# Kernel optimization log

Measured on AMD Instinct MI355X. Metric: run time of the kernel, lower is better.

Reference implementation:

```python
import jax, jax.numpy as jnp
import numpy as np

B, N, C, C_OUT, E = 8, 1024, 256, 256, 16384


def setup_inputs() -> dict:
    key = jax.random.key(0)
    k1, k2, k3 = jax.random.split(key, 3)
    x = jax.random.normal(k1, (B, N, C), dtype=jnp.float32)
    edge_index = jax.random.randint(k2, (2, E, B), 0, N)  # [2, E, B], values in [0, N)
    W = jax.random.normal(k3, (C_OUT, C), dtype=jnp.float32) * 0.02  # torch Linear weight [out, in]
    b = jnp.zeros((C_OUT,), dtype=jnp.float32)
    return {"x": x, "edge_index": edge_index, "W": W, "b": b}


def reference(x, edge_index, W, b):
    Bs, Nn, Cc = x.shape
    BN = Bs * Nn
    # Vectorized version of the per-batch python loop: offset each graph's
    # node indices into the big block-diagonal adjacency.
    offs = jnp.arange(Bs, dtype=edge_index.dtype) * Nn          # [B]
    src = (edge_index[0] + offs[None, :]).reshape(-1)           # [E*B]
    dst = (edge_index[1] + offs[None, :]).reshape(-1)           # [E*B]
    adj = jnp.zeros((BN, BN), dtype=x.dtype).at[src, dst].set(1.0)
    adj = adj + jnp.eye(BN, dtype=x.dtype)                      # self loops (adds on top, as in torch code)
    D = adj.sum(axis=1)                                         # [BN]
    d_inv_sqrt = jnp.where(D > 0, jax.lax.rsqrt(D), 0.0)        # pow(-0.5) with inf -> 0
    adj_n = d_inv_sqrt[:, None] * adj * d_inv_sqrt[None, :]     # D^-1/2 A D^-1/2
    h = adj_n @ x.reshape(BN, Cc)                               # [BN, C]
    out = h @ W.T + b                                           # Linear
    return out.reshape(Bs, Nn, -1)
```

## Files before the change

### kernel.cpp

```cpp
#include <hip/hip_runtime.h>
#include <stdint.h>

#define B_   8
#define N_   1024
#define C_   256
#define E_   16384
#define BN_  (B_ * N_)
#define NW_  (N_ / 32)
#define LIST_CAP 96

typedef __attribute__((ext_vector_type(8))) short bf16x8;
typedef __attribute__((ext_vector_type(4))) float f32x4;

static __device__ __forceinline__ short f32_to_bf16(float f) {
  uint32_t u = __float_as_uint(f);
  uint32_t r = (u + 0x7fffu + ((u >> 16) & 1u)) >> 16;
  return (short)r;
}
static __device__ __forceinline__ float bf16_to_f32(short s) {
  return __uint_as_float(((uint32_t)(uint16_t)s) << 16);
}

__global__ __launch_bounds__(256) void scatter_edges(
    const int* __restrict__ ei, uint32_t* __restrict__ mask) {
  int t = blockIdx.x * 256 + threadIdx.x;
  if (t >= E_ * B_) return;
  int b   = t & (B_ - 1);
  int src = ei[t];
  int dst = ei[E_ * B_ + t];
  int row = b * N_ + src;
  atomicOr(&mask[row * NW_ + (dst >> 5)], 1u << (dst & 31));
}

__global__ __launch_bounds__(256) void gemm_bf16x3(
    const float* __restrict__ X, const float* __restrict__ W,
    const uint32_t* __restrict__ mask, float* __restrict__ Z) {
  __shared__ __attribute__((aligned(16))) short Ah[64][40];
  __shared__ __attribute__((aligned(16))) short Al[64][40];
  __shared__ __attribute__((aligned(16))) short Bh[64][40];
  __shared__ __attribute__((aligned(16))) short Bl[64][40];
  __shared__ int   dpart[4][64];
  __shared__ float dinv_s[64];

  int t  = threadIdx.x;
  int m0 = blockIdx.x * 64;
  int n0 = blockIdx.y * 64;

  {
    int row = t & 63, part = t >> 6;
    const uint4* mp =
        (const uint4*)&mask[(size_t)(m0 + row) * NW_ + part * 8];
    uint4 a = mp[0], b = mp[1];
    dpart[part][row] = __popc(a.x) + __popc(a.y) + __popc(a.z) + __popc(a.w) +
                       __popc(b.x) + __popc(b.y) + __popc(b.z) + __popc(b.w);
  }
  __syncthreads();
  if (t < 64) {
    int d = dpart[0][t] + dpart[1][t] + dpart[2][t] + dpart[3][t] + 1;
    dinv_s[t] = rsqrtf((float)d);
  }

  int lr = t >> 2;
  int lc = (t & 3) * 8;
  int wv = t >> 6;
  int ln = t & 63;
  int lm = ln & 15;
  int qd = ln >> 4;

  f32x4 acc[4];
#pragma unroll
  for (int i = 0; i < 4; i++) acc[i] = (f32x4){0.f, 0.f, 0.f, 0.f};

  for (int k0 = 0; k0 < C_; k0 += 32) {
    const float* xr = &X[(size_t)(m0 + lr) * C_ + k0 + lc];
    const float* wr = &W[(size_t)(n0 + lr) * C_ + k0 + lc];
    float xv[8], wv8[8];
    *(float4*)&xv[0] = *(const float4*)&xr[0];
    *(float4*)&xv[4] = *(const float4*)&xr[4];
    *(float4*)&wv8[0] = *(const float4*)&wr[0];
    *(float4*)&wv8[4] = *(const float4*)&wr[4];
    bf16x8 xh, xl, wh, wl;
#pragma unroll
    for (int j = 0; j < 8; j++) {
      short h = f32_to_bf16(xv[j]);
      xh[j] = h;
      xl[j] = f32_to_bf16(xv[j] - bf16_to_f32(h));
      short g = f32_to_bf16(wv8[j]);
      wh[j] = g;
      wl[j] = f32_to_bf16(wv8[j] - bf16_to_f32(g));
    }
    __syncthreads();
    *(bf16x8*)&Ah[lr][lc] = xh;
    *(bf16x8*)&Al[lr][lc] = xl;
    *(bf16x8*)&Bh[lr][lc] = wh;
    *(bf16x8*)&Bl[lr][lc] = wl;
    __syncthreads();

    bf16x8 ah = *(const bf16x8*)&Ah[16 * wv + lm][qd * 8];
    bf16x8 al = *(const bf16x8*)&Al[16 * wv + lm][qd * 8];
#pragma unroll
    for (int nt = 0; nt < 4; nt++) {
      bf16x8 bh = *(const bf16x8*)&Bh[nt * 16 + lm][qd * 8];
      bf16x8 bl = *(const bf16x8*)&Bl[nt * 16 + lm][qd * 8];
      acc[nt] = __builtin_amdgcn_mfma_f32_16x16x32_bf16(ah, bh, acc[nt], 0, 0, 0);
      acc[nt] = __builtin_amdgcn_mfma_f32_16x16x32_bf16(ah, bl, acc[nt], 0, 0, 0);
      acc[nt] = __builtin_amdgcn_mfma_f32_16x16x32_bf16(al, bh, acc[nt], 0, 0, 0);
    }
  }
  __syncthreads();

  float di[4];
#pragma unroll
  for (int r = 0; r < 4; r++) di[r] = dinv_s[16 * wv + qd * 4 + r];
#pragma unroll
  for (int nt = 0; nt < 4; nt++) {
#pragma unroll
    for (int r = 0; r < 4; r++) {
      int m = m0 + 16 * wv + qd * 4 + r;
      int n = n0 + nt * 16 + lm;
      Z[(size_t)m * C_ + n] = di[r] * acc[nt][r];
    }
  }
}

__global__ __launch_bounds__(256) void aggregate(
    const uint32_t* __restrict__ mask, const float* __restrict__ Z,
    const float* __restrict__ bias, float* __restrict__ out) {
  __shared__ uint16_t lists[4][LIST_CAP];

  int blk   = blockIdx.x;
  int batch = blk & 7;
  int group = blk >> 3;
  int wv    = threadIdx.x >> 6;
  int ln    = threadIdx.x & 63;
  int loc   = group * 4 + wv;
  int node  = batch * N_ + loc;
  int c4    = ln * 4;

  uint32_t bits = (ln < NW_) ? mask[(size_t)node * NW_ + ln] : 0u;
  int cnt = __popc(bits);
  int pfx = cnt;
#pragma unroll
  for (int off = 1; off < 64; off <<= 1) {
    int v = __shfl_up(pfx, off);
    if (ln >= off) pfx += v;
  }
  int total = __shfl(pfx, 63);
  pfx -= cnt;
  uint16_t* lst = lists[wv];
  int o = pfx, jb = ln * 32;
  while (bits) {
    int j = __ffs(bits) - 1;
    bits &= bits - 1;
    lst[o++] = (uint16_t)(jb + j);
  }
  if (ln == 0) {
    int dd = total;
    while (dd & 3) lst[dd++] = 0;
  }

  const float* zb = Z + (size_t)batch * N_ * C_;
  float4 acc = *(const float4*)&zb[(size_t)loc * C_ + c4];

  for (int k = 0; k < total; k += 4) {
    ushort4 n4 = *(const ushort4*)&lst[k];
    float4 z0 = *(const float4*)&zb[(size_t)n4.x * C_ + c4];
    float4 z1 = *(const float4*)&zb[(size_t)n4.y * C_ + c4];
    float4 z2 = *(const float4*)&zb[(size_t)n4.z * C_ + c4];
    float4 z3 = *(const float4*)&zb[(size_t)n4.w * C_ + c4];
    float w1 = (k + 1 < total) ? 1.f : 0.f;
    float w2 = (k + 2 < total) ? 1.f : 0.f;
    float w3 = (k + 3 < total) ? 1.f : 0.f;
    acc.x += z0.x; acc.y += z0.y; acc.z += z0.z; acc.w += z0.w;
    acc.x += w1 * z1.x; acc.y += w1 * z1.y; acc.z += w1 * z1.z; acc.w += w1 * z1.w;
    acc.x += w2 * z2.x; acc.y += w2 * z2.y; acc.z += w2 * z2.z; acc.w += w2 * z2.w;
    acc.x += w3 * z3.x; acc.y += w3 * z3.y; acc.z += w3 * z3.z; acc.w += w3 * z3.w;
  }

  float di = rsqrtf((float)(total + 1));
  float4 bb = *(const float4*)&bias[c4];
  float4 o4;
  o4.x = di * acc.x + bb.x;
  o4.y = di * acc.y + bb.y;
  o4.z = di * acc.z + bb.z;
  o4.w = di * acc.w + bb.w;
  *(float4*)&out[(size_t)node * C_ + c4] = o4;
}

extern "C" void kernel_launch(void* const* d_in, const int* in_sizes, int n_in,
                              void* d_out, int out_size, void* d_ws,
                              size_t ws_size, hipStream_t stream) {
  const float* x    = (const float*)d_in[0];
  const int*   ei   = (const int*)d_in[1];
  const float* W    = (const float*)d_in[2];
  const float* bias = (const float*)d_in[3];
  float*       out  = (float*)d_out;

  char* ws = (char*)d_ws;
  uint32_t* mask = (uint32_t*)(ws + 0x000000);
  float*    Z    = (float*)   (ws + 0x100000);

  hipMemsetAsync(mask, 0, (size_t)BN_ * NW_ * 4, stream);

  scatter_edges<<<(E_ * B_) / 256, 256, 0, stream>>>(ei, mask);
  gemm_bf16x3<<<dim3(BN_ / 64, C_ / 64), 256, 0, stream>>>(x, W, mask, Z);
  aggregate<<<BN_ / 4, 256, 0, stream>>>(mask, Z, bias, out);
}
```

Baseline: 97.17 us.

## Preload whole W tile to LDS once and load X fragments directly into registers

The GEMM kernel now converts the block's full 64x256 slice of W into bf16 hi/lo parts and stores it in shared memory once, in a k-chunk-major layout. Each wave then loads its X fragments straight from global memory into MFMA operand registers, which removes the A tiles from LDS and the two barriers per k-step. The grid becomes 1D with a remapped block index so that blocks sharing an X row tile are interleaved. LDS use grows to about 64KB per block, which can cut occupancy, and X reads are now uncoalesced per-lane 32-byte loads.

```diff
diff --git a/kernel.cpp b/kernel.cpp
--- a/kernel.cpp
+++ b/kernel.cpp
@@ -35,16 +35,17 @@
 __global__ __launch_bounds__(256) void gemm_bf16x3(
     const float* __restrict__ X, const float* __restrict__ W,
     const uint32_t* __restrict__ mask, float* __restrict__ Z) {
-  __shared__ __attribute__((aligned(16))) short Ah[64][40];
-  __shared__ __attribute__((aligned(16))) short Al[64][40];
-  __shared__ __attribute__((aligned(16))) short Bh[64][40];
-  __shared__ __attribute__((aligned(16))) short Bl[64][40];
+  __shared__ __attribute__((aligned(16))) short Bh[32][64][8];
+  __shared__ __attribute__((aligned(16))) short Bl[32][64][8];
   __shared__ int   dpart[4][64];
   __shared__ float dinv_s[64];
 
-  int t  = threadIdx.x;
-  int m0 = blockIdx.x * 64;
-  int n0 = blockIdx.y * 64;
+  int t   = threadIdx.x;
+  int id  = blockIdx.x;
+  int loc = id >> 3;
+  int mt  = (id & 7) * 16 + (loc >> 2);
+  int m0  = mt * 64;
+  int n0  = (loc & 3) * 64;
 
   {
     int row = t & 63, part = t >> 6;
@@ -54,54 +55,60 @@
     dpart[part][row] = __popc(a.x) + __popc(a.y) + __popc(a.z) + __popc(a.w) +
                        __popc(b.x) + __popc(b.y) + __popc(b.z) + __popc(b.w);
   }
+
+#pragma unroll
+  for (int i = 0; i < 8; i++) {
+    int row = t & 63;
+    int ch  = (t >> 6) * 8 + i;
+    const float* wr = &W[(size_t)(n0 + row) * C_ + ch * 8];
+    float w8[8];
+    *(float4*)&w8[0] = *(const float4*)&wr[0];
+    *(float4*)&w8[4] = *(const float4*)&wr[4];
+    bf16x8 wh, wl;
+#pragma unroll
+    for (int j = 0; j < 8; j++) {
+      short h = f32_to_bf16(w8[j]);
+      wh[j] = h;
+      wl[j] = f32_to_bf16(w8[j] - bf16_to_f32(h));
+    }
+    *(bf16x8*)&Bh[ch][row][0] = wh;
+    *(bf16x8*)&Bl[ch][row][0] = wl;
+  }
   __syncthreads();
+
   if (t < 64) {
     int d = dpart[0][t] + dpart[1][t] + dpart[2][t] + dpart[3][t] + 1;
     dinv_s[t] = rsqrtf((float)d);
   }
 
-  int lr = t >> 2;
-  int lc = (t & 3) * 8;
   int wv = t >> 6;
   int ln = t & 63;
   int lm = ln & 15;
   int qd = ln >> 4;
 
+  const float* xr = &X[(size_t)(m0 + 16 * wv + lm) * C_ + qd * 8];
+
   f32x4 acc[4];
 #pragma unroll
   for (int i = 0; i < 4; i++) acc[i] = (f32x4){0.f, 0.f, 0.f, 0.f};
 
+#pragma unroll
   for (int k0 = 0; k0 < C_; k0 += 32) {
-    const float* xr = &X[(size_t)(m0 + lr) * C_ + k0 + lc];
-    const float* wr = &W[(size_t)(n0 + lr) * C_ + k0 + lc];
-    float xv[8], wv8[8];
-    *(float4*)&xv[0] = *(const float4*)&xr[0];
-    *(float4*)&xv[4] = *(const float4*)&xr[4];
-    *(float4*)&wv8[0] = *(const float4*)&wr[0];
-    *(float4*)&wv8[4] = *(const float4*)&wr[4];
-    bf16x8 xh, xl, wh, wl;
+    float xv[8];
+    *(float4*)&xv[0] = *(const float4*)&xr[k0];
+    *(float4*)&xv[4] = *(const float4*)&xr[k0 + 4];
+    bf16x8 ah, al;
 #pragma unroll
     for (int j = 0; j < 8; j++) {
       short h = f32_to_bf16(xv[j]);
-      xh[j] = h;
-      xl[j] = f32_to_bf16(xv[j] - bf16_to_f32(h));
-      short g = f32_to_bf16(wv8[j]);
-      wh[j] = g;
-      wl[j] = f32_to_bf16(wv8[j] - bf16_to_f32(g));
-    }
-    __syncthreads();
-    *(bf16x8*)&Ah[lr][lc] = xh;
-    *(bf16x8*)&Al[lr][lc] = xl;
-    *(bf16x8*)&Bh[lr][lc] = wh;
-    *(bf16x8*)&Bl[lr][lc] = wl;
-    __syncthreads();
-
-    bf16x8 ah = *(const bf16x8*)&Ah[16 * wv + lm][qd * 8];
-    bf16x8 al = *(const bf16x8*)&Al[16 * wv + lm][qd * 8];
+      ah[j] = h;
+      al[j] = f32_to_bf16(xv[j] - bf16_to_f32(h));
+    }
+    int cq = (k0 >> 3) + qd;
 #pragma unroll
     for (int nt = 0; nt < 4; nt++) {
-      bf16x8 bh = *(const bf16x8*)&Bh[nt * 16 + lm][qd * 8];
-      bf16x8 bl = *(const bf16x8*)&Bl[nt * 16 + lm][qd * 8];
+      bf16x8 bh = *(const bf16x8*)&Bh[cq][nt * 16 + lm][0];
+      bf16x8 bl = *(const bf16x8*)&Bl[cq][nt * 16 + lm][0];
       acc[nt] = __builtin_amdgcn_mfma_f32_16x16x32_bf16(ah, bh, acc[nt], 0, 0, 0);
       acc[nt] = __builtin_amdgcn_mfma_f32_16x16x32_bf16(ah, bl, acc[nt], 0, 0, 0);
       acc[nt] = __builtin_amdgcn_mfma_f32_16x16x32_bf16(al, bh, acc[nt], 0, 0, 0);
@@ -203,6 +210,6 @@
   hipMemsetAsync(mask, 0, (size_t)BN_ * NW_ * 4, stream);
 
   scatter_edges<<<(E_ * B_) / 256, 256, 0, stream>>>(ei, mask);
-  gemm_bf16x3<<<dim3(BN_ / 64, C_ / 64), 256, 0, stream>>>(x, W, mask, Z);
+  gemm_bf16x3<<<512, 256, 0, stream>>>(x, W, mask, Z);
   aggregate<<<BN_ / 4, 256, 0, stream>>>(mask, Z, bias, out);
 }
```

After: 95.46 us, median of 2. No clear change (-1.8%).
